# Kernel optimization log

Hardware: AMD Instinct MI355X
Metric: run time of the kernel (lower is better)

## Reference

```python
import jax, jax.numpy as jnp
import numpy as np

N_NODES = 100000
N_EDGES = 20000
NNZ = 600000
N_GRAPHS = 64
IN_C, HID_C, OUT_C = 128, 128, 16


def setup_inputs() -> dict:
    key = jax.random.key(0)
    ks = jax.random.split(key, 10)
    x = jax.random.normal(ks[0], (N_NODES, IN_C), dtype=jnp.float32)
    node_idx = jax.random.randint(ks[1], (NNZ,), 0, N_NODES)
    edge_idx = jax.random.randint(ks[2], (NNZ,), 0, N_EDGES)
    batch = jnp.sort(jax.random.randint(ks[3], (N_NODES,), 0, N_GRAPHS))
    s1 = 1.0 / np.sqrt(IN_C)
    s2 = 1.0 / np.sqrt(HID_C)
    W1 = jax.random.uniform(ks[4], (IN_C, HID_C), jnp.float32, -s1, s1)
    b1 = jnp.zeros((HID_C,), jnp.float32)
    W2 = jax.random.uniform(ks[5], (HID_C, HID_C), jnp.float32, -s2, s2)
    b2 = jnp.zeros((HID_C,), jnp.float32)
    Wfc = jax.random.uniform(ks[6], (HID_C, OUT_C), jnp.float32, -s2, s2)
    bfc = jax.random.uniform(ks[7], (OUT_C,), jnp.float32, -s2, s2)
    return {"x": x, "node_idx": node_idx, "edge_idx": edge_idx, "batch": batch,
            "W1": W1, "b1": b1, "W2": W2, "b2": b2, "Wfc": Wfc, "bfc": bfc}


def hypergraph_conv(x, node_idx, edge_idx, W, b):
    # x' = D^{-1} H B^{-1} H^T (x W) + b   (unit hyperedge weights)
    x = x @ W  # lin has bias=False in PyG HypergraphConv
    ones = jnp.ones((node_idx.shape[0],), x.dtype)
    De = jax.ops.segment_sum(ones, edge_idx, num_segments=N_EDGES)   # hyperedge degree
    Dn = jax.ops.segment_sum(ones, node_idx, num_segments=N_NODES)  # node degree
    Binv = jnp.where(De > 0, 1.0 / De, 0.0)[:, None]
    Dinv = jnp.where(Dn > 0, 1.0 / Dn, 0.0)[:, None]
    # node -> hyperedge aggregation
    e = jax.ops.segment_sum(x[node_idx], edge_idx, num_segments=N_EDGES) * Binv
    # hyperedge -> node aggregation
    out = jax.ops.segment_sum(e[edge_idx], node_idx, num_segments=N_NODES) * Dinv
    return out + b


def reference(x, node_idx, edge_idx, batch, W1, b1, W2, b2, Wfc, bfc):
    h = jax.nn.relu(hypergraph_conv(x, node_idx, edge_idx, W1, b1))
    h = jax.nn.relu(hypergraph_conv(h, node_idx, edge_idx, W2, b2))
    # global mean pool over graphs
    cnt = jax.ops.segment_sum(jnp.ones((N_NODES,), h.dtype), batch, num_segments=N_GRAPHS)
    pooled = jax.ops.segment_sum(h, batch, num_segments=N_GRAPHS) / jnp.maximum(cnt, 1.0)[:, None]
    logits = pooled @ Wfc + bfc
    return jax.nn.log_softmax(logits, axis=1)
```

## Files before the change

### kernel.cpp

```cpp
#include <hip/hip_runtime.h>

#define N_NODES  100000
#define N_EDGES  20000
#define NNZ_     600000
#define N_GRAPHS 64
#define C_       128

typedef unsigned short ushort_t;
typedef unsigned int   uint_t;
typedef unsigned char  uchar_t;
typedef __attribute__((ext_vector_type(8))) short bf16x8;
typedef __attribute__((ext_vector_type(8))) unsigned short u16x8;
typedef __attribute__((ext_vector_type(4))) float f32x4;
typedef __attribute__((ext_vector_type(2))) float f32x2;

__device__ __forceinline__ ushort_t f2bf(float f) {
    uint_t u = __float_as_uint(f);
    u += 0x7fffu + ((u >> 16) & 1u);
    return (ushort_t)(u >> 16);
}
__device__ __forceinline__ uint_t pkbf(float lo, float hi) {
    return ((uint_t)f2bf(hi) << 16) | f2bf(lo);
}


#define SORT_ITEMS 2048
#define BKT_CAP    16384
#define NBKT_E     40
#define NBKT_N     49
#define SB_        ((NNZ_ + SORT_ITEMS - 1) / SORT_ITEMS)
#define CONV_XBLKS 6250

__global__ __launch_bounds__(256) void scatter_conv(const int* __restrict__ node_idx,
                                                    const int* __restrict__ edge_idx,
                                                    int* __restrict__ bcur,
                                                    int2* __restrict__ stage_e,
                                                    int2* __restrict__ stage_n,
                                                    const float* __restrict__ X, uint_t* __restrict__ X8,
                                                    const float* __restrict__ W1, const float* __restrict__ W2,
                                                    ushort_t* __restrict__ WT1, ushort_t* __restrict__ WT2) {
    __shared__ int cnt[NBKT_N];
    __shared__ int base[NBKT_N];
    __shared__ int gbase[NBKT_N];
    __shared__ int2 buf[SORT_ITEMS];
    int t = threadIdx.x;
    int bxx = blockIdx.x;

    if (bxx >= SB_) {
        int bx = bxx - SB_;
        if (bx < CONV_XBLKS) {
            size_t c = (size_t)bx * 256 + t;
            size_t bb = c * 8;
            if (bb >= (size_t)N_NODES * C_) return;
            float4 f0 = *(const float4*)(X + bb);
            float4 f1 = *(const float4*)(X + bb + 4);
            uint_t w0 = 0, w1 = 0;
            w0 = __builtin_amdgcn_cvt_pk_fp8_f32(f0.x, f0.y, w0, 0);
            w0 = __builtin_amdgcn_cvt_pk_fp8_f32(f0.z, f0.w, w0, 1);
            w1 = __builtin_amdgcn_cvt_pk_fp8_f32(f1.x, f1.y, w1, 0);
            w1 = __builtin_amdgcn_cvt_pk_fp8_f32(f1.z, f1.w, w1, 1);
            uint2 o; o.x = w0; o.y = w1;
            *(uint2*)(X8 + c * 2) = o;
        } else {
            bx -= CONV_XBLKS;
            const float* W = (bx < 64) ? W1 : W2;
            ushort_t* WT   = (bx < 64) ? WT1 : WT2;
            int idx = (bx & 63) * 256 + t;
            int nn = idx >> 7, k = idx & 127;
            WT[nn * 128 + k] = f2bf(W[k * 128 + nn]);
        }
        return;
    }

    int start = bxx * SORT_ITEMS;
    int nitems = min(SORT_ITEMS, NNZ_ - start);

    int ek[8], nk[8];
    #pragma unroll
    for (int j = 0; j < 8; j++) {
        int i = t + j * 256;
        if (i < nitems) { ek[j] = edge_idx[start + i]; nk[j] = node_idx[start + i]; }
    }

    #pragma unroll
    for (int side = 0; side < 2; side++) {
        const int SHIFT = side ? 11 : 9;
        const int NBKT  = side ? NBKT_N : NBKT_E;
        int2* stage = side ? stage_n : stage_e;
        int*  bc    = bcur + side * 64;

        if (side) __syncthreads();
        for (int i = t; i < NBKT; i += 256) cnt[i] = 0;
        __syncthreads();

        int rank[8], bkt[8];
        #pragma unroll
        for (int j = 0; j < 8; j++) {
            int i = t + j * 256;
            if (i < nitems) {
                int key = side ? nk[j] : ek[j];
                bkt[j]  = key >> SHIFT;
                rank[j] = atomicAdd(&cnt[bkt[j]], 1);
            }
        }
        __syncthreads();
        if (t < 64) {
            int v = (t < NBKT) ? cnt[t] : 0;
            int s = v;
            #pragma unroll
            for (int o = 1; o < 64; o <<= 1) { int u = __shfl_up(s, o); if (t >= o) s += u; }
            if (t < NBKT) base[t] = s - v;
        }
        __syncthreads();
        if (t < NBKT) {
            int c = cnt[t];
            gbase[t] = t * BKT_CAP + ((c > 0) ? atomicAdd(&bc[t], c) : 0);
        }
        #pragma unroll
        for (int j = 0; j < 8; j++) {
            int i = t + j * 256;
            if (i < nitems) {
                int key = side ? nk[j] : ek[j];
                int val = side ? ek[j] : nk[j];
                buf[base[bkt[j]] + rank[j]] = make_int2(key, val);
            }
        }
        __syncthreads();
        for (int i = t; i < nitems; i += 256) {
            int2 p = buf[i];
            int b = p.x >> SHIFT;
            stage[gbase[b] + (i - base[b])] = p;
        }
    }
}

__global__ __launch_bounds__(1024) void bucket_build(const int2* __restrict__ stage_e,
                                                     const int2* __restrict__ stage_n,
                                                     const int* __restrict__ bcur,
                                                     int* __restrict__ ecnt, int* __restrict__ ncnt,
                                                     int* __restrict__ eoffs, int* __restrict__ noffs,
                                                     float* __restrict__ binv, float* __restrict__ dinv,
                                                     int* __restrict__ csr_en, int* __restrict__ csr_ne) {
    __shared__ int hist[2048];
    __shared__ int offs[2048];
    __shared__ int wsum[16];
    __shared__ int sbase;
    int t = threadIdx.x;
    int bx = blockIdx.x;
    const int2* sb; int* cnt; int* koffs; float* inv; int* csr;
    const int* bc; int b, width, nkeys, nb, k0;
    if (bx < NBKT_E) {
        b = bx; bc = bcur;
        sb = stage_e + (size_t)b * BKT_CAP; cnt = ecnt; koffs = eoffs; inv = binv; csr = csr_en;
        k0 = b << 9; width = 512; nkeys = N_EDGES; nb = NBKT_E;
    } else {
        b = bx - NBKT_E; bc = bcur + 64;
        sb = stage_n + (size_t)b * BKT_CAP; cnt = ncnt; koffs = noffs; inv = dinv; csr = csr_ne;
        k0 = b << 11; width = 2048; nkeys = N_NODES; nb = NBKT_N;
    }
    int n = bc[b];
    if (t < 64) {
        int v = (t < nb) ? bc[t] : 0;
        int s = v;
        #pragma unroll
        for (int o = 1; o < 64; o <<= 1) { int u = __shfl_up(s, o); if (t >= o) s += u; }
        if (t == b) sbase = s - v;
    }
    for (int i = t; i < width; i += 1024) hist[i] = 0;
    __syncthreads();
    for (int i = t; i < n; i += 1024) atomicAdd(&hist[sb[i].x - k0], 1);
    __syncthreads();
    int e0 = 0, e1 = 0;
    if (2 * t < width) { e0 = hist[2 * t]; e1 = hist[2 * t + 1]; }
    int s = e0 + e1;
    int lane = t & 63, wv = t >> 6;
    int sc = s;
    #pragma unroll
    for (int o = 1; o < 64; o <<= 1) { int u = __shfl_up(sc, o); if (lane >= o) sc += u; }
    if (lane == 63) wsum[wv] = sc;
    __syncthreads();
    if (t < 16) {
        int v = wsum[t];
        int s2 = v;
        #pragma unroll
        for (int o = 1; o < 16; o <<= 1) { int u = __shfl_up(s2, o); if (t >= o) s2 += u; }
        wsum[t] = s2 - v;
    }
    __syncthreads();
    if (2 * t < width) {
        int excl = (sc - s) + wsum[wv];
        offs[2 * t]     = excl;
        offs[2 * t + 1] = excl + e0;
    }
    __syncthreads();
    int base_g = sbase;
    for (int i = t; i < width; i += 1024) {
        int k = k0 + i;
        if (k < nkeys) {
            int c = hist[i];
            cnt[k]   = c;
            koffs[k] = base_g + offs[i];
            inv[k]   = (c > 0) ? 1.0f / (float)c : 0.0f;
        }
    }
    __syncthreads();
    for (int i = t; i < n; i += 1024) {
        int2 p = sb[i];
        int pos = atomicAdd(&offs[p.x - k0], 1);
        csr[base_g + pos] = p.y;
    }
}


__global__ __launch_bounds__(256) void gemm_mfma(const ushort_t* __restrict__ Ab,
                                                 const ushort_t* __restrict__ WT,
                                                 uchar_t* __restrict__ C8, int M) {
    __shared__ __align__(16) ushort_t Wl[128 * 128];
    __shared__ __align__(16) ushort_t Al[64 * 128];
    int t = threadIdx.x;
    int r0 = blockIdx.x * 64;

    const uint4* WTg = (const uint4*)WT;
    #pragma unroll
    for (int i = 0; i < 8; i++) {
        int c = i * 256 + t;
        int row = c >> 4, colel = (c & 15) * 8;
        *(uint4*)&Wl[row * 128 + (colel ^ ((row & 7) << 3))] = WTg[c];
    }
    #pragma unroll
    for (int i = 0; i < 4; i++) {
        int c = i * 256 + t;
        int row = c >> 4;
        int colel = (c & 15) * 8;
        int gr = r0 + row; if (gr >= M) gr = M - 1;
        u16x8 v = *(const u16x8*)(Ab + (size_t)gr * 128 + colel);
        *(u16x8*)&Al[row * 128 + (colel ^ ((row & 7) << 3))] = v;
    }
    __syncthreads();

    int lane = t & 63, wid = t >> 6;
    int arow = wid * 16 + (lane & 15);
    int kq = lane >> 4;
    f32x4 acc[8] = {};

    #pragma unroll
    for (int ks = 0; ks < 4; ks++) {
        int colel = ks * 32 + kq * 8;
        bf16x8 a = *(const bf16x8*)&Al[arow * 128 + (colel ^ ((arow & 7) << 3))];
        #pragma unroll
        for (int nt = 0; nt < 8; nt++) {
            int wr = nt * 16 + (lane & 15);
            bf16x8 b = *(const bf16x8*)&Wl[wr * 128 + (colel ^ ((wr & 7) << 3))];
            acc[nt] = __builtin_amdgcn_mfma_f32_16x16x32_bf16(a, b, acc[nt], 0, 0, 0);
        }
    }

    __syncthreads();
    uchar_t* Cl = (uchar_t*)Al;
    #pragma unroll
    for (int nt = 0; nt < 8; nt++) {
        int col = nt * 16 + (lane & 15);
        #pragma unroll
        for (int j = 0; j < 4; j++) {
            int rl = wid * 16 + kq * 4 + j;
            uint_t p = __builtin_amdgcn_cvt_pk_fp8_f32(acc[nt][j], acc[nt][j], 0, 0);
            Cl[rl * 128 + col] = (uchar_t)(p & 0xff);
        }
    }
    __syncthreads();
    int rows_here = min(64, M - r0);
    uint4* dst = (uint4*)(C8 + (size_t)r0 * 128);
    const uint4* src = (const uint4*)Cl;
    for (int c = t; c < rows_here * 8; c += 256) dst[c] = src[c];
}


__device__ __forceinline__ void acc16(uint4 v, float* a) {
    f32x2 p0 = __builtin_amdgcn_cvt_pk_f32_fp8(v.x, 0);
    f32x2 p1 = __builtin_amdgcn_cvt_pk_f32_fp8(v.x, 1);
    f32x2 p2 = __builtin_amdgcn_cvt_pk_f32_fp8(v.y, 0);
    f32x2 p3 = __builtin_amdgcn_cvt_pk_f32_fp8(v.y, 1);
    f32x2 p4 = __builtin_amdgcn_cvt_pk_f32_fp8(v.z, 0);
    f32x2 p5 = __builtin_amdgcn_cvt_pk_f32_fp8(v.z, 1);
    f32x2 p6 = __builtin_amdgcn_cvt_pk_f32_fp8(v.w, 0);
    f32x2 p7 = __builtin_amdgcn_cvt_pk_f32_fp8(v.w, 1);
    a[0] += p0.x;  a[1] += p0.y;  a[2] += p1.x;  a[3] += p1.y;
    a[4] += p2.x;  a[5] += p2.y;  a[6] += p3.x;  a[7] += p3.y;
    a[8] += p4.x;  a[9] += p4.y;  a[10] += p5.x; a[11] += p5.y;
    a[12] += p6.x; a[13] += p6.y; a[14] += p7.x; a[15] += p7.y;
}

__global__ __launch_bounds__(256) void gather_edges8(const uint4* __restrict__ X,
                                                     const int* __restrict__ csr,
                                                     const int* __restrict__ off, const int* __restrict__ cnt,
                                                     const float* __restrict__ binv,
                                                     ushort_t* __restrict__ E) {
    int g = (blockIdx.x * blockDim.x + threadIdx.x) >> 3;
    int l = threadIdx.x & 7;
    if (g >= N_EDGES) return;
    int s = off[g], n = cnt[g];
    float a[16] = {};
    int i = 0;
    for (; i + 4 <= n; i += 4) {
        int r0 = csr[s + i], r1 = csr[s + i + 1], r2 = csr[s + i + 2], r3 = csr[s + i + 3];
        uint4 v0 = X[(size_t)r0 * 8 + l];
        uint4 v1 = X[(size_t)r1 * 8 + l];
        uint4 v2 = X[(size_t)r2 * 8 + l];
        uint4 v3 = X[(size_t)r3 * 8 + l];
        acc16(v0, a); acc16(v1, a); acc16(v2, a); acc16(v3, a);
    }
    for (; i < n; i++) {
        uint4 v = X[(size_t)csr[s + i] * 8 + l];
        acc16(v, a);
    }
    float sc = binv[g];
    uint4 o0, o1;
    o0.x = pkbf(a[0] * sc,  a[1] * sc);
    o0.y = pkbf(a[2] * sc,  a[3] * sc);
    o0.z = pkbf(a[4] * sc,  a[5] * sc);
    o0.w = pkbf(a[6] * sc,  a[7] * sc);
    o1.x = pkbf(a[8] * sc,  a[9] * sc);
    o1.y = pkbf(a[10] * sc, a[11] * sc);
    o1.z = pkbf(a[12] * sc, a[13] * sc);
    o1.w = pkbf(a[14] * sc, a[15] * sc);
    uint4* dst = (uint4*)(E + (size_t)g * 128) + l * 2;
    dst[0] = o0; dst[1] = o1;
}

__global__ __launch_bounds__(256) void gather_nodes8(const uint4* __restrict__ F,
                                                     const int* __restrict__ csr,
                                                     const int* __restrict__ off, const int* __restrict__ cnt,
                                                     const float* __restrict__ dinv,
                                                     const float* __restrict__ bias,
                                                     uint4* __restrict__ Y) {
    int g = (blockIdx.x * blockDim.x + threadIdx.x) >> 3;
    int l = threadIdx.x & 7;
    if (g >= N_NODES) return;
    int s = off[g], n = cnt[g];
    float a[16] = {};
    int i = 0;
    for (; i + 4 <= n; i += 4) {
        int r0 = csr[s + i], r1 = csr[s + i + 1], r2 = csr[s + i + 2], r3 = csr[s + i + 3];
        uint4 v0 = F[(size_t)r0 * 8 + l];
        uint4 v1 = F[(size_t)r1 * 8 + l];
        uint4 v2 = F[(size_t)r2 * 8 + l];
        uint4 v3 = F[(size_t)r3 * 8 + l];
        acc16(v0, a); acc16(v1, a); acc16(v2, a); acc16(v3, a);
    }
    for (; i < n; i++) {
        uint4 v = F[(size_t)csr[s + i] * 8 + l];
        acc16(v, a);
    }
    float sc = dinv[g];
    const float4* bb = (const float4*)bias + l * 4;
    float4 b0 = bb[0], b1 = bb[1], b2 = bb[2], b3 = bb[3];
    float r[16];
    r[0]  = fmaxf(a[0]  * sc + b0.x, 0.f);
    r[1]  = fmaxf(a[1]  * sc + b0.y, 0.f);
    r[2]  = fmaxf(a[2]  * sc + b0.z, 0.f);
    r[3]  = fmaxf(a[3]  * sc + b0.w, 0.f);
    r[4]  = fmaxf(a[4]  * sc + b1.x, 0.f);
    r[5]  = fmaxf(a[5]  * sc + b1.y, 0.f);
    r[6]  = fmaxf(a[6]  * sc + b1.z, 0.f);
    r[7]  = fmaxf(a[7]  * sc + b1.w, 0.f);
    r[8]  = fmaxf(a[8]  * sc + b2.x, 0.f);
    r[9]  = fmaxf(a[9]  * sc + b2.y, 0.f);
    r[10] = fmaxf(a[10] * sc + b2.z, 0.f);
    r[11] = fmaxf(a[11] * sc + b2.w, 0.f);
    r[12] = fmaxf(a[12] * sc + b3.x, 0.f);
    r[13] = fmaxf(a[13] * sc + b3.y, 0.f);
    r[14] = fmaxf(a[14] * sc + b3.z, 0.f);
    r[15] = fmaxf(a[15] * sc + b3.w, 0.f);
    uint_t w0 = __builtin_amdgcn_cvt_pk_fp8_f32(r[0],  r[1],  0, 0);
    w0 = __builtin_amdgcn_cvt_pk_fp8_f32(r[2],  r[3],  w0, 1);
    uint_t w1 = __builtin_amdgcn_cvt_pk_fp8_f32(r[4],  r[5],  0, 0);
    w1 = __builtin_amdgcn_cvt_pk_fp8_f32(r[6],  r[7],  w1, 1);
    uint_t w2 = __builtin_amdgcn_cvt_pk_fp8_f32(r[8],  r[9],  0, 0);
    w2 = __builtin_amdgcn_cvt_pk_fp8_f32(r[10], r[11], w2, 1);
    uint_t w3 = __builtin_amdgcn_cvt_pk_fp8_f32(r[12], r[13], 0, 0);
    w3 = __builtin_amdgcn_cvt_pk_fp8_f32(r[14], r[15], w3, 1);
    uint4 o; o.x = w0; o.y = w1; o.z = w2; o.w = w3;
    Y[(size_t)g * 8 + l] = o;
}


#define POOL_BLOCKS 1024

__global__ __launch_bounds__(256) void pool_kernel8(const ushort_t* __restrict__ H,
                                                    const int* __restrict__ batch,
                                                    float* __restrict__ P) {
    int wgid = blockIdx.x * 4 + (threadIdx.x >> 6);
    int lane = threadIdx.x & 63;
    const int NW = POOL_BLOCKS * 4;
    const int per = (N_NODES + NW - 1) / NW;
    int r0 = wgid * per;
    int r1 = min(r0 + per, N_NODES);
    if (r0 >= r1) return;
    float ax = 0.f, ay = 0.f;
    int g = batch[r0];
    int hiw = lane & 1;
    for (int r = r0; r < r1; r++) {
        int gr = batch[r];
        if (gr != g) {
            atomicAdd(&P[g * C_ + lane * 2],     ax);
            atomicAdd(&P[g * C_ + lane * 2 + 1], ay);
            ax = 0.f; ay = 0.f; g = gr;
        }
        uint_t v = ((const uint_t*)H)[(size_t)r * 32 + (lane >> 1)];
        f32x2 p = hiw ? __builtin_amdgcn_cvt_pk_f32_fp8(v, 1)
                      : __builtin_amdgcn_cvt_pk_f32_fp8(v, 0);
        ax += p.x; ay += p.y;
    }
    atomicAdd(&P[g * C_ + lane * 2],     ax);
    atomicAdd(&P[g * C_ + lane * 2 + 1], ay);
}

__device__ __forceinline__ int lower_bound_dev(const int* __restrict__ a, int n, int key) {
    int lo = 0, hi = n;
    while (lo < hi) { int mid = (lo + hi) >> 1; if (a[mid] < key) lo = mid + 1; else hi = mid; }
    return lo;
}

__global__ __launch_bounds__(1024) void final_kernel(const float* __restrict__ P, const int* __restrict__ batch,
                                                     const float* __restrict__ Wfc, const float* __restrict__ bfc,
                                                     float* __restrict__ out) {
    int t = threadIdx.x;
    int r = t >> 4, c = t & 15;
    int lo = lower_bound_dev(batch, N_NODES, r);
    int hi = lower_bound_dev(batch, N_NODES, r + 1);
    float cnt = (float)((hi - lo) > 0 ? (hi - lo) : 1);
    float acc = 0.f;
    #pragma unroll 8
    for (int k = 0; k < C_; k++) acc += P[r * C_ + k] * Wfc[k * 16 + c];
    float logit = acc / cnt + bfc[c];
    __shared__ float l[N_GRAPHS][16];
    l[r][c] = logit;
    __syncthreads();
    float m = -1e30f;
    #pragma unroll
    for (int k = 0; k < 16; k++) m = fmaxf(m, l[r][k]);
    float sum = 0.f;
    #pragma unroll
    for (int k = 0; k < 16; k++) sum += expf(l[r][k] - m);
    out[t] = logit - m - logf(sum);
}


extern "C" void kernel_launch(void* const* d_in, const int* in_sizes, int n_in,
                              void* d_out, int out_size, void* d_ws, size_t ws_size,
                              hipStream_t stream) {
    const float* x        = (const float*)d_in[0];
    const int*   node_idx = (const int*)  d_in[1];
    const int*   edge_idx = (const int*)  d_in[2];
    const int*   batch    = (const int*)  d_in[3];
    const float* W1       = (const float*)d_in[4];
    const float* b1       = (const float*)d_in[5];
    const float* W2       = (const float*)d_in[6];
    const float* b2       = (const float*)d_in[7];
    const float* Wfc      = (const float*)d_in[8];
    const float* bfc      = (const float*)d_in[9];
    float* out = (float*)d_out;

    char* ws = (char*)d_ws;
    size_t off = 0;
    auto alloc = [&](size_t bytes) -> char* {
        off = (off + 255) & ~(size_t)255;
        char* p = ws + off;
        off += bytes;
        return p;
    };

    uint_t* x8     = (uint_t*)  alloc((size_t)N_NODES * C_);
    uint_t* h8     = (uint_t*)  alloc((size_t)N_NODES * C_);
    ushort_t* Eb   = (ushort_t*)alloc((size_t)N_EDGES * C_ * 2);
    uchar_t* Fb8   = (uchar_t*) alloc((size_t)N_EDGES * C_);
    ushort_t* wt1  = (ushort_t*)alloc((size_t)C_ * C_ * 2);
    ushort_t* wt2  = (ushort_t*)alloc((size_t)C_ * C_ * 2);
    int2*  stage_e = (int2*) alloc((size_t)NBKT_E * BKT_CAP * 8);
    int2*  stage_n = (int2*) alloc((size_t)NBKT_N * BKT_CAP * 8);
    int*   bcur   = (int*)  alloc((size_t)128 * 4);
    float* pooled = (float*)alloc((size_t)N_GRAPHS * C_ * 4);
    char*  zend   = ws + off;
    int*   ecnt   = (int*)  alloc((size_t)N_EDGES * 4);
    int*   ncnt   = (int*)  alloc((size_t)N_NODES * 4);
    int*   eoffs  = (int*)  alloc((size_t)N_EDGES * 4);
    int*   noffs  = (int*)  alloc((size_t)N_NODES * 4);
    int*   csr_en = (int*)  alloc((size_t)NNZ_ * 4);
    int*   csr_ne = (int*)  alloc((size_t)NNZ_ * 4);
    float* binv   = (float*)alloc((size_t)N_EDGES * 4);
    float* dinv   = (float*)alloc((size_t)N_NODES * 4);

    (void)hipMemsetAsync((void*)bcur, 0, (size_t)(zend - (char*)bcur), stream);

    scatter_conv<<<SB_ + CONV_XBLKS + 128, 256, 0, stream>>>(
        node_idx, edge_idx, bcur, stage_e, stage_n, x, x8, W1, W2, wt1, wt2);
    bucket_build<<<NBKT_E + NBKT_N, 1024, 0, stream>>>(
        stage_e, stage_n, bcur, ecnt, ncnt, eoffs, noffs, binv, dinv, csr_en, csr_ne);

    const int GEB = (N_EDGES + 63) / 64;
    gather_edges8<<<N_EDGES * 8 / 256, 256, 0, stream>>>((const uint4*)x8, csr_en, eoffs, ecnt, binv, Eb);
    gemm_mfma<<<GEB, 256, 0, stream>>>(Eb, wt1, Fb8, N_EDGES);
    gather_nodes8<<<N_NODES * 8 / 256, 256, 0, stream>>>((const uint4*)Fb8, csr_ne, noffs, ncnt, dinv, b1,
                                                         (uint4*)h8);
    gather_edges8<<<N_EDGES * 8 / 256, 256, 0, stream>>>((const uint4*)h8, csr_en, eoffs, ecnt, binv, Eb);
    gemm_mfma<<<GEB, 256, 0, stream>>>(Eb, wt2, Fb8, N_EDGES);
    gather_nodes8<<<N_NODES * 8 / 256, 256, 0, stream>>>((const uint4*)Fb8, csr_ne, noffs, ncnt, dinv, b2,
                                                         (uint4*)x8);
    pool_kernel8<<<POOL_BLOCKS, 256, 0, stream>>>((const ushort_t*)x8, batch, pooled);
    final_kernel<<<1, 1024, 0, stream>>>(pooled, batch, Wfc, bfc, out);
}
```

Before: 159.9 us.

## Switch edge GEMM to FP8 MFMA, unroll edge gather, fuse pool with head

Switches the edge-feature intermediate and transposed weights from bf16 to fp8 and uses the fp8 16x16x32 MFMA, halving staging bytes and LDS traffic in the GEMM. Adds an 8-way unrolled loop in the edge gather to keep more loads in flight. Fuses the pooling and final log-softmax kernels with a last-block-done counter, removing one launch. FP8 for activations and weights lowers accuracy further, and the last-block pattern adds a global atomic and fence per block.

```diff
diff --git a/kernel.cpp b/kernel.cpp
--- a/kernel.cpp
+++ b/kernel.cpp
@@ -9,8 +9,6 @@
 typedef unsigned short ushort_t;
 typedef unsigned int   uint_t;
 typedef unsigned char  uchar_t;
-typedef __attribute__((ext_vector_type(8))) short bf16x8;
-typedef __attribute__((ext_vector_type(8))) unsigned short u16x8;
 typedef __attribute__((ext_vector_type(4))) float f32x4;
 typedef __attribute__((ext_vector_type(2))) float f32x2;
 
@@ -18,9 +16,6 @@
     uint_t u = __float_as_uint(f);
     u += 0x7fffu + ((u >> 16) & 1u);
     return (ushort_t)(u >> 16);
-}
-__device__ __forceinline__ uint_t pkbf(float lo, float hi) {
-    return ((uint_t)f2bf(hi) << 16) | f2bf(lo);
 }
 
 
@@ -30,6 +25,7 @@
 #define NBKT_N     49
 #define SB_        ((NNZ_ + SORT_ITEMS - 1) / SORT_ITEMS)
 #define CONV_XBLKS 6250
+#define CONV_WBLKS 64
 
 __global__ __launch_bounds__(256) void scatter_conv(const int* __restrict__ node_idx,
                                                     const int* __restrict__ edge_idx,
@@ -38,7 +34,7 @@
                                                     int2* __restrict__ stage_n,
                                                     const float* __restrict__ X, uint_t* __restrict__ X8,
                                                     const float* __restrict__ W1, const float* __restrict__ W2,
-                                                    ushort_t* __restrict__ WT1, ushort_t* __restrict__ WT2) {
+                                                    uchar_t* __restrict__ WT1, uchar_t* __restrict__ WT2) {
     __shared__ int cnt[NBKT_N];
     __shared__ int base[NBKT_N];
     __shared__ int gbase[NBKT_N];
@@ -63,11 +59,14 @@
             *(uint2*)(X8 + c * 2) = o;
         } else {
             bx -= CONV_XBLKS;
-            const float* W = (bx < 64) ? W1 : W2;
-            ushort_t* WT   = (bx < 64) ? WT1 : WT2;
-            int idx = (bx & 63) * 256 + t;
-            int nn = idx >> 7, k = idx & 127;
-            WT[nn * 128 + k] = f2bf(W[k * 128 + nn]);
+            const float* W = (bx < 32) ? W1 : W2;
+            uchar_t* WT    = (bx < 32) ? WT1 : WT2;
+            int idx = (bx & 31) * 256 + t;
+            int n = idx >> 6, k2 = (idx & 63) * 2;
+            float a = W[k2 * 128 + n];
+            float b = W[(k2 + 1) * 128 + n];
+            uint_t p = __builtin_amdgcn_cvt_pk_fp8_f32(a, b, 0, 0);
+            *(ushort_t*)(WT + n * 128 + k2) = (ushort_t)(p & 0xffff);
         }
         return;
     }
@@ -212,29 +211,28 @@
 }
 
 
-__global__ __launch_bounds__(256) void gemm_mfma(const ushort_t* __restrict__ Ab,
-                                                 const ushort_t* __restrict__ WT,
-                                                 uchar_t* __restrict__ C8, int M) {
-    __shared__ __align__(16) ushort_t Wl[128 * 128];
-    __shared__ __align__(16) ushort_t Al[64 * 128];
+__global__ __launch_bounds__(256) void gemm_mfma8(const uchar_t* __restrict__ A8,
+                                                  const uchar_t* __restrict__ WT8,
+                                                  uchar_t* __restrict__ C8, int M) {
+    __shared__ __align__(16) uchar_t Wl[128 * 128];
+    __shared__ __align__(16) uchar_t Al[64 * 128];
     int t = threadIdx.x;
     int r0 = blockIdx.x * 64;
 
-    const uint4* WTg = (const uint4*)WT;
-    #pragma unroll
-    for (int i = 0; i < 8; i++) {
-        int c = i * 256 + t;
-        int row = c >> 4, colel = (c & 15) * 8;
-        *(uint4*)&Wl[row * 128 + (colel ^ ((row & 7) << 3))] = WTg[c];
-    }
+    const uint4* WTg = (const uint4*)WT8;
     #pragma unroll
     for (int i = 0; i < 4; i++) {
         int c = i * 256 + t;
-        int row = c >> 4;
-        int colel = (c & 15) * 8;
+        int row = c >> 3, col16 = (c & 7) * 16;
+        *(uint4*)&Wl[row * 128 + (col16 ^ ((row & 7) << 4))] = WTg[c];
+    }
+    #pragma unroll
+    for (int i = 0; i < 2; i++) {
+        int c = i * 256 + t;
+        int row = c >> 3, col16 = (c & 7) * 16;
         int gr = r0 + row; if (gr >= M) gr = M - 1;
-        u16x8 v = *(const u16x8*)(Ab + (size_t)gr * 128 + colel);
-        *(u16x8*)&Al[row * 128 + (colel ^ ((row & 7) << 3))] = v;
+        uint4 v = *(const uint4*)(A8 + (size_t)gr * 128 + col16);
+        *(uint4*)&Al[row * 128 + (col16 ^ ((row & 7) << 4))] = v;
     }
     __syncthreads();
 
@@ -245,18 +243,18 @@
 
     #pragma unroll
     for (int ks = 0; ks < 4; ks++) {
-        int colel = ks * 32 + kq * 8;
-        bf16x8 a = *(const bf16x8*)&Al[arow * 128 + (colel ^ ((arow & 7) << 3))];
+        int colb = ks * 32 + kq * 8;
+        long a = *(const long*)&Al[arow * 128 + (colb ^ ((arow & 7) << 4))];
         #pragma unroll
         for (int nt = 0; nt < 8; nt++) {
             int wr = nt * 16 + (lane & 15);
-            bf16x8 b = *(const bf16x8*)&Wl[wr * 128 + (colel ^ ((wr & 7) << 3))];
-            acc[nt] = __builtin_amdgcn_mfma_f32_16x16x32_bf16(a, b, acc[nt], 0, 0, 0);
-        }
-    }
-
-    __syncthreads();
-    uchar_t* Cl = (uchar_t*)Al;
+            long b = *(const long*)&Wl[wr * 128 + (colb ^ ((wr & 7) << 4))];
+            acc[nt] = __builtin_amdgcn_mfma_f32_16x16x32_fp8_fp8(a, b, acc[nt], 0, 0, 0);
+        }
+    }
+
+    __syncthreads();
+    uchar_t* Cl = Al;
     #pragma unroll
     for (int nt = 0; nt < 8; nt++) {
         int col = nt * 16 + (lane & 15);
@@ -290,17 +288,44 @@
     a[12] += p6.x; a[13] += p6.y; a[14] += p7.x; a[15] += p7.y;
 }
 
+__device__ __forceinline__ uint4 pack16(const float* r) {
+    uint_t w0 = __builtin_amdgcn_cvt_pk_fp8_f32(r[0],  r[1],  0, 0);
+    w0 = __builtin_amdgcn_cvt_pk_fp8_f32(r[2],  r[3],  w0, 1);
+    uint_t w1 = __builtin_amdgcn_cvt_pk_fp8_f32(r[4],  r[5],  0, 0);
+    w1 = __builtin_amdgcn_cvt_pk_fp8_f32(r[6],  r[7],  w1, 1);
+    uint_t w2 = __builtin_amdgcn_cvt_pk_fp8_f32(r[8],  r[9],  0, 0);
+    w2 = __builtin_amdgcn_cvt_pk_fp8_f32(r[10], r[11], w2, 1);
+    uint_t w3 = __builtin_amdgcn_cvt_pk_fp8_f32(r[12], r[13], 0, 0);
+    w3 = __builtin_amdgcn_cvt_pk_fp8_f32(r[14], r[15], w3, 1);
+    uint4 o; o.x = w0; o.y = w1; o.z = w2; o.w = w3;
+    return o;
+}
+
 __global__ __launch_bounds__(256) void gather_edges8(const uint4* __restrict__ X,
                                                      const int* __restrict__ csr,
                                                      const int* __restrict__ off, const int* __restrict__ cnt,
                                                      const float* __restrict__ binv,
-                                                     ushort_t* __restrict__ E) {
+                                                     uint4* __restrict__ E8) {
     int g = (blockIdx.x * blockDim.x + threadIdx.x) >> 3;
     int l = threadIdx.x & 7;
     if (g >= N_EDGES) return;
     int s = off[g], n = cnt[g];
     float a[16] = {};
     int i = 0;
+    for (; i + 8 <= n; i += 8) {
+        int r0 = csr[s + i],     r1 = csr[s + i + 1], r2 = csr[s + i + 2], r3 = csr[s + i + 3];
+        int r4 = csr[s + i + 4], r5 = csr[s + i + 5], r6 = csr[s + i + 6], r7 = csr[s + i + 7];
+        uint4 v0 = X[(size_t)r0 * 8 + l];
+        uint4 v1 = X[(size_t)r1 * 8 + l];
+        uint4 v2 = X[(size_t)r2 * 8 + l];
+        uint4 v3 = X[(size_t)r3 * 8 + l];
+        uint4 v4 = X[(size_t)r4 * 8 + l];
+        uint4 v5 = X[(size_t)r5 * 8 + l];
+        uint4 v6 = X[(size_t)r6 * 8 + l];
+        uint4 v7 = X[(size_t)r7 * 8 + l];
+        acc16(v0, a); acc16(v1, a); acc16(v2, a); acc16(v3, a);
+        acc16(v4, a); acc16(v5, a); acc16(v6, a); acc16(v7, a);
+    }
     for (; i + 4 <= n; i += 4) {
         int r0 = csr[s + i], r1 = csr[s + i + 1], r2 = csr[s + i + 2], r3 = csr[s + i + 3];
         uint4 v0 = X[(size_t)r0 * 8 + l];
@@ -314,17 +339,10 @@
         acc16(v, a);
     }
     float sc = binv[g];
-    uint4 o0, o1;
-    o0.x = pkbf(a[0] * sc,  a[1] * sc);
-    o0.y = pkbf(a[2] * sc,  a[3] * sc);
-    o0.z = pkbf(a[4] * sc,  a[5] * sc);
-    o0.w = pkbf(a[6] * sc,  a[7] * sc);
-    o1.x = pkbf(a[8] * sc,  a[9] * sc);
-    o1.y = pkbf(a[10] * sc, a[11] * sc);
-    o1.z = pkbf(a[12] * sc, a[13] * sc);
-    o1.w = pkbf(a[14] * sc, a[15] * sc);
-    uint4* dst = (uint4*)(E + (size_t)g * 128) + l * 2;
-    dst[0] = o0; dst[1] = o1;
+    float r[16];
+    #pragma unroll
+    for (int j = 0; j < 16; j++) r[j] = a[j] * sc;
+    E8[(size_t)g * 8 + l] = pack16(r);
 }
 
 __global__ __launch_bounds__(256) void gather_nodes8(const uint4* __restrict__ F,
@@ -371,78 +389,87 @@
     r[13] = fmaxf(a[13] * sc + b3.y, 0.f);
     r[14] = fmaxf(a[14] * sc + b3.z, 0.f);
     r[15] = fmaxf(a[15] * sc + b3.w, 0.f);
-    uint_t w0 = __builtin_amdgcn_cvt_pk_fp8_f32(r[0],  r[1],  0, 0);
-    w0 = __builtin_amdgcn_cvt_pk_fp8_f32(r[2],  r[3],  w0, 1);
-    uint_t w1 = __builtin_amdgcn_cvt_pk_fp8_f32(r[4],  r[5],  0, 0);
-    w1 = __builtin_amdgcn_cvt_pk_fp8_f32(r[6],  r[7],  w1, 1);
-    uint_t w2 = __builtin_amdgcn_cvt_pk_fp8_f32(r[8],  r[9],  0, 0);
-    w2 = __builtin_amdgcn_cvt_pk_fp8_f32(r[10], r[11], w2, 1);
-    uint_t w3 = __builtin_amdgcn_cvt_pk_fp8_f32(r[12], r[13], 0, 0);
-    w3 = __builtin_amdgcn_cvt_pk_fp8_f32(r[14], r[15], w3, 1);
-    uint4 o; o.x = w0; o.y = w1; o.z = w2; o.w = w3;
-    Y[(size_t)g * 8 + l] = o;
+    Y[(size_t)g * 8 + l] = pack16(r);
 }
 
 
 #define POOL_BLOCKS 1024
 
-__global__ __launch_bounds__(256) void pool_kernel8(const ushort_t* __restrict__ H,
-                                                    const int* __restrict__ batch,
-                                                    float* __restrict__ P) {
-    int wgid = blockIdx.x * 4 + (threadIdx.x >> 6);
-    int lane = threadIdx.x & 63;
+__device__ __forceinline__ int lower_bound_dev(const int* __restrict__ a, int n, int key) {
+    int lo = 0, hi = n;
+    while (lo < hi) { int mid = (lo + hi) >> 1; if (a[mid] < key) lo = mid + 1; else hi = mid; }
+    return lo;
+}
+
+__global__ __launch_bounds__(256) void pool_head(const ushort_t* __restrict__ H,
+                                                 const int* __restrict__ batch,
+                                                 float* __restrict__ P,
+                                                 int* __restrict__ done,
+                                                 const float* __restrict__ Wfc,
+                                                 const float* __restrict__ bfc,
+                                                 float* __restrict__ out) {
+    int t = threadIdx.x;
+    int wgid = blockIdx.x * 4 + (t >> 6);
+    int lane = t & 63;
     const int NW = POOL_BLOCKS * 4;
     const int per = (N_NODES + NW - 1) / NW;
     int r0 = wgid * per;
     int r1 = min(r0 + per, N_NODES);
-    if (r0 >= r1) return;
-    float ax = 0.f, ay = 0.f;
-    int g = batch[r0];
-    int hiw = lane & 1;
-    for (int r = r0; r < r1; r++) {
-        int gr = batch[r];
-        if (gr != g) {
-            atomicAdd(&P[g * C_ + lane * 2],     ax);
-            atomicAdd(&P[g * C_ + lane * 2 + 1], ay);
-            ax = 0.f; ay = 0.f; g = gr;
-        }
-        uint_t v = ((const uint_t*)H)[(size_t)r * 32 + (lane >> 1)];
-        f32x2 p = hiw ? __builtin_amdgcn_cvt_pk_f32_fp8(v, 1)
-                      : __builtin_amdgcn_cvt_pk_f32_fp8(v, 0);
-        ax += p.x; ay += p.y;
-    }
-    atomicAdd(&P[g * C_ + lane * 2],     ax);
-    atomicAdd(&P[g * C_ + lane * 2 + 1], ay);
-}
-
-__device__ __forceinline__ int lower_bound_dev(const int* __restrict__ a, int n, int key) {
-    int lo = 0, hi = n;
-    while (lo < hi) { int mid = (lo + hi) >> 1; if (a[mid] < key) lo = mid + 1; else hi = mid; }
-    return lo;
-}
-
-__global__ __launch_bounds__(1024) void final_kernel(const float* __restrict__ P, const int* __restrict__ batch,
-                                                     const float* __restrict__ Wfc, const float* __restrict__ bfc,
-                                                     float* __restrict__ out) {
-    int t = threadIdx.x;
-    int r = t >> 4, c = t & 15;
-    int lo = lower_bound_dev(batch, N_NODES, r);
-    int hi = lower_bound_dev(batch, N_NODES, r + 1);
-    float cnt = (float)((hi - lo) > 0 ? (hi - lo) : 1);
-    float acc = 0.f;
-    #pragma unroll 8
-    for (int k = 0; k < C_; k++) acc += P[r * C_ + k] * Wfc[k * 16 + c];
-    float logit = acc / cnt + bfc[c];
+    if (r0 < r1) {
+        float ax = 0.f, ay = 0.f;
+        int g = batch[r0];
+        int hiw = lane & 1;
+        for (int r = r0; r < r1; r++) {
+            int gr = batch[r];
+            if (gr != g) {
+                atomicAdd(&P[g * C_ + lane * 2],     ax);
+                atomicAdd(&P[g * C_ + lane * 2 + 1], ay);
+                ax = 0.f; ay = 0.f; g = gr;
+            }
+            uint_t v = ((const uint_t*)H)[(size_t)r * 32 + (lane >> 1)];
+            f32x2 p = hiw ? __builtin_amdgcn_cvt_pk_f32_fp8(v, 1)
+                          : __builtin_amdgcn_cvt_pk_f32_fp8(v, 0);
+            ax += p.x; ay += p.y;
+        }
+        atomicAdd(&P[g * C_ + lane * 2],     ax);
+        atomicAdd(&P[g * C_ + lane * 2 + 1], ay);
+    }
+    __threadfence();
+    __shared__ int lastf;
+    __syncthreads();
+    if (t == 0) lastf = (atomicAdd(done, 1) == POOL_BLOCKS - 1) ? 1 : 0;
+    __syncthreads();
+    if (!lastf) return;
+    __threadfence();
+
     __shared__ float l[N_GRAPHS][16];
-    l[r][c] = logit;
-    __syncthreads();
-    float m = -1e30f;
-    #pragma unroll
-    for (int k = 0; k < 16; k++) m = fmaxf(m, l[r][k]);
-    float sum = 0.f;
-    #pragma unroll
-    for (int k = 0; k < 16; k++) sum += expf(l[r][k] - m);
-    out[t] = logit - m - logf(sum);
+    float logit[4];
+    #pragma unroll
+    for (int j = 0; j < 4; j++) {
+        int idx = t + j * 256;
+        int r = idx >> 4, c = idx & 15;
+        int lo = lower_bound_dev(batch, N_NODES, r);
+        int hi = lower_bound_dev(batch, N_NODES, r + 1);
+        float cntf = (float)((hi - lo) > 0 ? (hi - lo) : 1);
+        float acc = 0.f;
+        #pragma unroll 8
+        for (int k = 0; k < C_; k++) acc += P[r * C_ + k] * Wfc[k * 16 + c];
+        logit[j] = acc / cntf + bfc[c];
+        l[r][c] = logit[j];
+    }
+    __syncthreads();
+    #pragma unroll
+    for (int j = 0; j < 4; j++) {
+        int idx = t + j * 256;
+        int r = idx >> 4;
+        float m = -1e30f;
+        #pragma unroll
+        for (int k = 0; k < 16; k++) m = fmaxf(m, l[r][k]);
+        float sum = 0.f;
+        #pragma unroll
+        for (int k = 0; k < 16; k++) sum += expf(l[r][k] - m);
+        out[idx] = logit[j] - m - logf(sum);
+    }
 }
 
 
@@ -472,13 +499,14 @@
 
     uint_t* x8     = (uint_t*)  alloc((size_t)N_NODES * C_);
     uint_t* h8     = (uint_t*)  alloc((size_t)N_NODES * C_);
-    ushort_t* Eb   = (ushort_t*)alloc((size_t)N_EDGES * C_ * 2);
+    uchar_t* Eb8   = (uchar_t*) alloc((size_t)N_EDGES * C_);
     uchar_t* Fb8   = (uchar_t*) alloc((size_t)N_EDGES * C_);
-    ushort_t* wt1  = (ushort_t*)alloc((size_t)C_ * C_ * 2);
-    ushort_t* wt2  = (ushort_t*)alloc((size_t)C_ * C_ * 2);
+    uchar_t* wt1   = (uchar_t*) alloc((size_t)C_ * C_);
+    uchar_t* wt2   = (uchar_t*) alloc((size_t)C_ * C_);
     int2*  stage_e = (int2*) alloc((size_t)NBKT_E * BKT_CAP * 8);
     int2*  stage_n = (int2*) alloc((size_t)NBKT_N * BKT_CAP * 8);
     int*   bcur   = (int*)  alloc((size_t)128 * 4);
+    int*   done   = (int*)  alloc((size_t)64 * 4);
     float* pooled = (float*)alloc((size_t)N_GRAPHS * C_ * 4);
     char*  zend   = ws + off;
     int*   ecnt   = (int*)  alloc((size_t)N_EDGES * 4);
@@ -492,20 +520,21 @@
 
     (void)hipMemsetAsync((void*)bcur, 0, (size_t)(zend - (char*)bcur), stream);
 
-    scatter_conv<<<SB_ + CONV_XBLKS + 128, 256, 0, stream>>>(
+    scatter_conv<<<SB_ + CONV_XBLKS + CONV_WBLKS, 256, 0, stream>>>(
         node_idx, edge_idx, bcur, stage_e, stage_n, x, x8, W1, W2, wt1, wt2);
     bucket_build<<<NBKT_E + NBKT_N, 1024, 0, stream>>>(
         stage_e, stage_n, bcur, ecnt, ncnt, eoffs, noffs, binv, dinv, csr_en, csr_ne);
 
     const int GEB = (N_EDGES + 63) / 64;
-    gather_edges8<<<N_EDGES * 8 / 256, 256, 0, stream>>>((const uint4*)x8, csr_en, eoffs, ecnt, binv, Eb);
-    gemm_mfma<<<GEB, 256, 0, stream>>>(Eb, wt1, Fb8, N_EDGES);
+    gather_edges8<<<N_EDGES * 8 / 256, 256, 0, stream>>>((const uint4*)x8, csr_en, eoffs, ecnt, binv,
+                                                         (uint4*)Eb8);
+    gemm_mfma8<<<GEB, 256, 0, stream>>>(Eb8, wt1, Fb8, N_EDGES);
     gather_nodes8<<<N_NODES * 8 / 256, 256, 0, stream>>>((const uint4*)Fb8, csr_ne, noffs, ncnt, dinv, b1,
                                                          (uint4*)h8);
-    gather_edges8<<<N_EDGES * 8 / 256, 256, 0, stream>>>((const uint4*)h8, csr_en, eoffs, ecnt, binv, Eb);
-    gemm_mfma<<<GEB, 256, 0, stream>>>(Eb, wt2, Fb8, N_EDGES);
+    gather_edges8<<<N_EDGES * 8 / 256, 256, 0, stream>>>((const uint4*)h8, csr_en, eoffs, ecnt, binv,
+                                                         (uint4*)Eb8);
+    gemm_mfma8<<<GEB, 256, 0, stream>>>(Eb8, wt2, Fb8, N_EDGES);
     gather_nodes8<<<N_NODES * 8 / 256, 256, 0, stream>>>((const uint4*)Fb8, csr_ne, noffs, ncnt, dinv, b2,
                                                          (uint4*)x8);
-    pool_kernel8<<<POOL_BLOCKS, 256, 0, stream>>>((const ushort_t*)x8, batch, pooled);
-    final_kernel<<<1, 1024, 0, stream>>>(pooled, batch, Wfc, bfc, out);
-}
+    pool_head<<<POOL_BLOCKS, 256, 0, stream>>>((const ushort_t*)x8, batch, pooled, done, Wfc, bfc, out);
+}
```

After: 249.9 us. 1.56x slower.
